# Kernel tuning notes

Hardware: AMD Instinct MI355X
Metric: run time of the kernel (lower is better)

Reference implementation:

```python
import jax, jax.numpy as jnp
import numpy as np

N_CLANS = 600   # rows of graph_fc.npy -> number of clan classes
MAX_F = 128     # max families per clan (padding size for stacked family heads)
B, L, D = 8192, 64, 256
NEG = -1e9      # mask value for padded family logits


def setup_inputs() -> dict:
    key = jax.random.key(0)
    k1, k2, k3, k4, k5, k6 = jax.random.split(key, 6)
    output = jax.random.normal(k1, (B, L, D), dtype=jnp.float32)
    fc = jax.random.randint(k2, (N_CLANS,), 1, MAX_F + 1)           # families per clan
    label_clan = jax.random.randint(k3, (B,), 0, N_CLANS)
    raw = jax.random.randint(k4, (B,), 0, MAX_F)
    label_family = raw % fc[label_clan]                              # valid family per sample
    W_clan = jax.random.normal(k5, (N_CLANS, D), dtype=jnp.float32) * 0.05
    b_clan = jnp.zeros((N_CLANS,), dtype=jnp.float32)
    W_fam = jax.random.normal(k6, (N_CLANS, MAX_F, D), dtype=jnp.float32) * 0.05
    b_fam = jnp.zeros((N_CLANS, MAX_F), dtype=jnp.float32)
    return {"output": output, "label_clan": label_clan, "label_family": label_family,
            "fc": fc, "W_clan": W_clan, "b_clan": b_clan, "W_fam": W_fam, "b_fam": b_fam}


def reference(output, label_clan, label_family, fc, W_clan, b_clan, W_fam, b_fam):
    x = output.mean(axis=1)                                          # [B, D]
    # clan CE loss (reduction='sum')
    logits_c = x @ W_clan.T + b_clan                                 # [B, N_CLANS]
    logp_c = jax.nn.log_softmax(logits_c, axis=-1)
    loss_clan = -jnp.take_along_axis(logp_c, label_clan[:, None], axis=1).sum()
    # routed per-sample family head: gather head weights by clan label
    Wg = W_fam[label_clan]                                           # [B, MAX_F, D]
    bg = b_fam[label_clan]                                           # [B, MAX_F]
    logits_f = jnp.einsum('bfd,bd->bf', Wg, x) + bg                  # [B, MAX_F]
    n_fam = fc[label_clan]                                           # [B]
    valid = jnp.arange(MAX_F)[None, :] < n_fam[:, None]              # mask padded families
    logits_f = jnp.where(valid, logits_f, NEG)
    logp_f = jax.nn.log_softmax(logits_f, axis=-1)
    nll = -jnp.take_along_axis(logp_f, label_family[:, None], axis=1)[:, 0]  # [B]
    active = n_fam > 1                                               # only clans with >1 family
    loss_family = jnp.where(active, nll, 0.0).sum()
    count = active.sum()
    loss = (loss_clan + loss_family) / (output.shape[0] + count)
    return loss
```

## Files before the change

kernel.cpp:

```cpp
#include <hip/hip_runtime.h>
#include <hip/hip_bf16.h>

#define B_SZ 8192
#define L_SZ 64
#define D_SZ 256
#define NC   600
#define MAXF 128
#define CAP  64

__global__ __launch_bounds__(256) void mean_kernel(const float* __restrict__ out,
                                                   float* __restrict__ x) {
    int gid = blockIdx.x * 256 + threadIdx.x;
    int b = gid >> 6, d4 = gid & 63;
    const float4* p = (const float4*)(out + (size_t)b * L_SZ * D_SZ) + d4;
    float4 acc = {0.f, 0.f, 0.f, 0.f};
#pragma unroll 8
    for (int l = 0; l < L_SZ; ++l) {
        float4 v = p[(size_t)l * (D_SZ / 4)];
        acc.x += v.x; acc.y += v.y; acc.z += v.z; acc.w += v.w;
    }
    const float s = 1.0f / 64.0f;
    acc.x *= s; acc.y *= s; acc.z *= s; acc.w *= s;
    ((float4*)(x + (size_t)b * D_SZ))[d4] = acc;
}

__global__ __launch_bounds__(256) void scatter_kernel(const int* __restrict__ label_clan,
                                                      const int* __restrict__ fc,
                                                      int* __restrict__ cnt,
                                                      int* __restrict__ list,
                                                      int* __restrict__ active_cnt) {
    int b = blockIdx.x * 256 + threadIdx.x;
    int cl = label_clan[b];
    int pos = atomicAdd(&cnt[cl], 1);
    if (pos < CAP) list[cl * CAP + pos] = b;
    int act = (fc[cl] > 1) ? 1 : 0;
    unsigned long long ball = __ballot(act);
    if ((threadIdx.x & 63) == 0) atomicAdd(active_cnt, (int)__popcll(ball));
}

#define CBM 32
__global__ __launch_bounds__(256) void clan_fused(const float* __restrict__ x,
                                                  const float* __restrict__ Wc,
                                                  const float* __restrict__ bc,
                                                  const int* __restrict__ label_clan,
                                                  float* __restrict__ acc_loss) {
    __shared__ float As[CBM][260];
    __shared__ float Bs[64][68];
    __shared__ float redm[CBM][16];
    __shared__ float mrow[CBM], srow[CBM], mnew[CBM], lablog[CBM];
    __shared__ int   labc[CBM];
    int t = threadIdx.x;
    int tx = t & 15, ty = t >> 4;
    int row0 = blockIdx.x * CBM;

#pragma unroll
    for (int rep = 0; rep < 8; ++rep) {
        int idx = t + rep * 256;
        int r = idx >> 6, c4 = idx & 63;
        *(float4*)&As[r][c4 * 4] = *(const float4*)(x + (size_t)(row0 + r) * D_SZ + c4 * 4);
    }
    if (t < CBM) {
        mrow[t] = -1e30f; srow[t] = 0.f; lablog[t] = 0.f;
        labc[t] = label_clan[row0 + t];
    }
    __syncthreads();

    for (int ct = 0; ct < 10; ++ct) {
        int c0 = ct * 64;
        float acc[2][4] = {};
        for (int k0 = 0; k0 < D_SZ; k0 += 64) {
            __syncthreads();
#pragma unroll
            for (int rep = 0; rep < 4; ++rep) {
                int idx = t + rep * 256;
                int col = idx >> 4, kq = idx & 15;
                int c = c0 + col;
                float4 v = {0.f, 0.f, 0.f, 0.f};
                if (c < NC) v = *(const float4*)(Wc + (size_t)c * D_SZ + k0 + kq * 4);
                *(float4*)&Bs[col][kq * 4] = v;
            }
            __syncthreads();
#pragma unroll
            for (int kk = 0; kk < 16; ++kk) {
                float4 a0 = *(float4*)&As[ty][k0 + kk * 4];
                float4 a1 = *(float4*)&As[ty + 16][k0 + kk * 4];
                float4 b[4];
#pragma unroll
                for (int j = 0; j < 4; ++j) b[j] = *(float4*)&Bs[tx + 16 * j][kk * 4];
#pragma unroll
                for (int j = 0; j < 4; ++j) {
                    acc[0][j] += a0.x * b[j].x + a0.y * b[j].y + a0.z * b[j].z + a0.w * b[j].w;
                    acc[1][j] += a1.x * b[j].x + a1.y * b[j].y + a1.z * b[j].z + a1.w * b[j].w;
                }
            }
        }
        float lg[2][4];
#pragma unroll
        for (int i = 0; i < 2; ++i) {
            int row = ty + 16 * i;
#pragma unroll
            for (int j = 0; j < 4; ++j) {
                int c = c0 + tx + 16 * j;
                float v = (c < NC) ? acc[i][j] + bc[c] : -1e30f;
                lg[i][j] = v;
                if (c < NC && c == labc[row]) lablog[row] = v;
            }
        }
#pragma unroll
        for (int i = 0; i < 2; ++i) {
            int row = ty + 16 * i;
            redm[row][tx] = fmaxf(fmaxf(lg[i][0], lg[i][1]), fmaxf(lg[i][2], lg[i][3]));
        }
        __syncthreads();
        if (t < CBM) {
            float tm = redm[t][0];
#pragma unroll
            for (int q = 1; q < 16; ++q) tm = fmaxf(tm, redm[t][q]);
            mnew[t] = fmaxf(mrow[t], tm);
        }
        __syncthreads();
#pragma unroll
        for (int i = 0; i < 2; ++i) {
            int row = ty + 16 * i;
            float mn = mnew[row];
            redm[row][tx] = __expf(lg[i][0] - mn) + __expf(lg[i][1] - mn)
                          + __expf(lg[i][2] - mn) + __expf(lg[i][3] - mn);
        }
        __syncthreads();
        if (t < CBM) {
            float s = 0.f;
#pragma unroll
            for (int q = 0; q < 16; ++q) s += redm[t][q];
            srow[t] = srow[t] * __expf(mrow[t] - mnew[t]) + s;
            mrow[t] = mnew[t];
        }
    }
    __syncthreads();
    if (t < 64) {
        float loss = 0.f;
        if (t < CBM) loss = __logf(srow[t]) + mrow[t] - lablog[t];
#pragma unroll
        for (int off = 16; off; off >>= 1) loss += __shfl_down(loss, off);
        if (t == 0) atomicAdd(acc_loss, loss);
    }
}

#define CHUNK 16
__global__ __launch_bounds__(256) void family_kernel(const float* __restrict__ x,
                                                     const float* __restrict__ Wf,
                                                     const float* __restrict__ bf,
                                                     const int* __restrict__ fc,
                                                     const int* __restrict__ cnt,
                                                     const int* __restrict__ list,
                                                     const int* __restrict__ label_family,
                                                     float* __restrict__ acc_loss) {
    int clan = blockIdx.x;
    int nf = fc[clan];
    if (nf <= 1) return;
    int n = min(cnt[clan], CAP);
    if (n == 0) return;
    __shared__ float sx[CHUNK][D_SZ];
    __shared__ float slog[CHUNK][MAXF];
    __shared__ int sb[CHUNK];
    __shared__ float wl[4];
    int t = threadIdx.x;
    int lane = t & 63, wid = t >> 6;
    const float* Wbase = Wf + (size_t)clan * MAXF * D_SZ;

    float wave_loss = 0.f;
    for (int s0 = 0; s0 < n; s0 += CHUNK) {
        int cn = min(CHUNK, n - s0);
        if (t < cn) sb[t] = list[clan * CAP + s0 + t];
        __syncthreads();
        for (int q = t; q < cn * (D_SZ / 4); q += 256) {
            int s = q >> 6, d4 = q & 63;
            ((float4*)sx[s])[d4] = ((const float4*)(x + (size_t)sb[s] * D_SZ))[d4];
        }
        __syncthreads();
        for (int f = wid; f < nf; f += 4) {
            float4 w = ((const float4*)(Wbase + (size_t)f * D_SZ))[lane];
            float bias = bf[clan * MAXF + f];
            for (int s = 0; s < cn; ++s) {
                float4 xv = ((float4*)sx[s])[lane];
                float p = w.x * xv.x + w.y * xv.y + w.z * xv.z + w.w * xv.w;
#pragma unroll
                for (int off = 32; off; off >>= 1) p += __shfl_down(p, off);
                if (lane == 0) slog[s][f] = p + bias;
            }
        }
        __syncthreads();
        for (int s = wid; s < cn; s += 4) {
            float v0 = (lane < nf) ? slog[s][lane] : -1e30f;
            float v1 = (lane + 64 < nf) ? slog[s][lane + 64] : -1e30f;
            float m = fmaxf(v0, v1);
#pragma unroll
            for (int off = 32; off; off >>= 1) m = fmaxf(m, __shfl_down(m, off));
            m = __shfl(m, 0);
            float e = 0.f;
            if (lane < nf) e += __expf(v0 - m);
            if (lane + 64 < nf) e += __expf(v1 - m);
#pragma unroll
            for (int off = 32; off; off >>= 1) e += __shfl_down(e, off);
            if (lane == 0) {
                int b = sb[s];
                int lf = label_family[b];
                wave_loss += __logf(e) + m - slog[s][lf];
            }
        }
        __syncthreads();
    }
    if (lane == 0) wl[wid] = wave_loss;
    __syncthreads();
    if (t == 0) {
        float v = wl[0] + wl[1] + wl[2] + wl[3];
        if (v != 0.f) atomicAdd(acc_loss, v);
    }
}

__global__ void finalize_kernel(const float* __restrict__ accs,
                                const int* __restrict__ active_cnt,
                                float* __restrict__ out) {
    out[0] = (accs[0] + accs[1]) / (8192.0f + (float)(*active_cnt));
}

extern "C" void kernel_launch(void* const* d_in, const int* in_sizes, int n_in,
                              void* d_out, int out_size, void* d_ws, size_t ws_size,
                              hipStream_t stream) {
    (void)in_sizes; (void)n_in; (void)out_size; (void)ws_size;
    const float* output       = (const float*)d_in[0];
    const int*   label_clan   = (const int*)d_in[1];
    const int*   label_family = (const int*)d_in[2];
    const int*   fc           = (const int*)d_in[3];
    const float* W_clan       = (const float*)d_in[4];
    const float* b_clan       = (const float*)d_in[5];
    const float* W_fam        = (const float*)d_in[6];
    const float* b_fam        = (const float*)d_in[7];
    float* out = (float*)d_out;

    char* ws = (char*)d_ws;
    const size_t OFF_X    = 0;
    const size_t OFF_CNT  = OFF_X + (size_t)B_SZ * D_SZ * 4;
    const size_t OFF_ACC  = OFF_CNT + 2560;
    const size_t OFF_LIST = OFF_ACC + 16;
    float* x      = (float*)(ws + OFF_X);
    int*   cnt    = (int*)(ws + OFF_CNT);
    float* accs   = (float*)(ws + OFF_ACC);
    int*   act    = (int*)(ws + OFF_ACC + 8);
    int*   list   = (int*)(ws + OFF_LIST);

    hipMemsetAsync(ws + OFF_CNT, 0, 2560 + 16, stream);

    mean_kernel<<<B_SZ * D_SZ / 4 / 256, 256, 0, stream>>>(output, x);
    scatter_kernel<<<B_SZ / 256, 256, 0, stream>>>(label_clan, fc, cnt, list, act);
    clan_fused<<<B_SZ / CBM, 256, 0, stream>>>(x, W_clan, b_clan, label_clan, accs);
    family_kernel<<<NC, 256, 0, stream>>>(x, W_fam, b_fam, fc, cnt, list, label_family, accs + 1);
    finalize_kernel<<<1, 1, 0, stream>>>(accs, act, out);
}
```

Before: 1.067 ms.

## Fuse scatter into mean kernel and run clan and family heads in one launch

```diff
diff --git a/kernel.cpp b/kernel.cpp
--- a/kernel.cpp
+++ b/kernel.cpp
@@ -7,10 +7,27 @@
 #define NC   600
 #define MAXF 128
 #define CAP  64
-
-__global__ __launch_bounds__(256) void mean_kernel(const float* __restrict__ out,
-                                                   float* __restrict__ x) {
-    int gid = blockIdx.x * 256 + threadIdx.x;
+#define CBM  32
+#define CHUNK 16
+
+__global__ __launch_bounds__(256) void mean_scatter(const float* __restrict__ out,
+                                                    float* __restrict__ x,
+                                                    const int* __restrict__ label_clan,
+                                                    const int* __restrict__ fc,
+                                                    int* __restrict__ cnt,
+                                                    int* __restrict__ list,
+                                                    int* __restrict__ active_cnt) {
+    int t = threadIdx.x;
+    if (blockIdx.x < 32) {
+        int b = blockIdx.x * 256 + t;
+        int cl = label_clan[b];
+        int pos = atomicAdd(&cnt[cl], 1);
+        if (pos < CAP) list[cl * CAP + pos] = b;
+        int act = (fc[cl] > 1) ? 1 : 0;
+        unsigned long long ball = __ballot(act);
+        if ((t & 63) == 0) atomicAdd(active_cnt, (int)__popcll(ball));
+    }
+    int gid = blockIdx.x * 256 + t;
     int b = gid >> 6, d4 = gid & 63;
     const float4* p = (const float4*)(out + (size_t)b * L_SZ * D_SZ) + d4;
     float4 acc = {0.f, 0.f, 0.f, 0.f};
@@ -24,34 +41,26 @@
     ((float4*)(x + (size_t)b * D_SZ))[d4] = acc;
 }
 
-__global__ __launch_bounds__(256) void scatter_kernel(const int* __restrict__ label_clan,
-                                                      const int* __restrict__ fc,
-                                                      int* __restrict__ cnt,
-                                                      int* __restrict__ list,
-                                                      int* __restrict__ active_cnt) {
-    int b = blockIdx.x * 256 + threadIdx.x;
-    int cl = label_clan[b];
-    int pos = atomicAdd(&cnt[cl], 1);
-    if (pos < CAP) list[cl * CAP + pos] = b;
-    int act = (fc[cl] > 1) ? 1 : 0;
-    unsigned long long ball = __ballot(act);
-    if ((threadIdx.x & 63) == 0) atomicAdd(active_cnt, (int)__popcll(ball));
-}
-
-#define CBM 32
-__global__ __launch_bounds__(256) void clan_fused(const float* __restrict__ x,
-                                                  const float* __restrict__ Wc,
-                                                  const float* __restrict__ bc,
-                                                  const int* __restrict__ label_clan,
-                                                  float* __restrict__ acc_loss) {
-    __shared__ float As[CBM][260];
-    __shared__ float Bs[64][68];
-    __shared__ float redm[CBM][16];
-    __shared__ float mrow[CBM], srow[CBM], mnew[CBM], lablog[CBM];
-    __shared__ int   labc[CBM];
+#define SMEM_FLOATS (53376 / 4)
+
+__device__ void clan_branch(float* smem, int blk,
+                            const float* __restrict__ x,
+                            const float* __restrict__ Wc,
+                            const float* __restrict__ bc,
+                            const int* __restrict__ label_clan,
+                            float* __restrict__ acc_loss) {
+    float (*As)[260] = (float(*)[260])smem;
+    float (*Bs)[68]  = (float(*)[68])(smem + 32 * 260);
+    float (*redm)[16] = (float(*)[16])(smem + 32 * 260 + 64 * 68);
+    float* mrow   = smem + 32 * 260 + 64 * 68 + 32 * 16;
+    float* srow   = mrow + 32;
+    float* mnew   = srow + 32;
+    float* lablog = mnew + 32;
+    int*   labc   = (int*)(lablog + 32);
+
     int t = threadIdx.x;
     int tx = t & 15, ty = t >> 4;
-    int row0 = blockIdx.x * CBM;
+    int row0 = blk * CBM;
 
 #pragma unroll
     for (int rep = 0; rep < 8; ++rep) {
@@ -145,24 +154,24 @@
     }
 }
 
-#define CHUNK 16
-__global__ __launch_bounds__(256) void family_kernel(const float* __restrict__ x,
-                                                     const float* __restrict__ Wf,
-                                                     const float* __restrict__ bf,
-                                                     const int* __restrict__ fc,
-                                                     const int* __restrict__ cnt,
-                                                     const int* __restrict__ list,
-                                                     const int* __restrict__ label_family,
-                                                     float* __restrict__ acc_loss) {
-    int clan = blockIdx.x;
+__device__ void family_branch(float* smem, int clan,
+                              const float* __restrict__ x,
+                              const float* __restrict__ Wf,
+                              const float* __restrict__ bf,
+                              const int* __restrict__ fc,
+                              const int* __restrict__ cnt,
+                              const int* __restrict__ list,
+                              const int* __restrict__ label_family,
+                              float* __restrict__ acc_loss) {
     int nf = fc[clan];
     if (nf <= 1) return;
     int n = min(cnt[clan], CAP);
     if (n == 0) return;
-    __shared__ float sx[CHUNK][D_SZ];
-    __shared__ float slog[CHUNK][MAXF];
-    __shared__ int sb[CHUNK];
-    __shared__ float wl[4];
+    float (*sx)[D_SZ]   = (float(*)[D_SZ])smem;
+    float (*slog)[MAXF] = (float(*)[MAXF])(smem + CHUNK * D_SZ);
+    int*   sb = (int*)(smem + CHUNK * D_SZ + CHUNK * MAXF);
+    float* wl = (float*)(sb + CHUNK);
+
     int t = threadIdx.x;
     int lane = t & 63, wid = t >> 6;
     const float* Wbase = Wf + (size_t)clan * MAXF * D_SZ;
@@ -214,6 +223,25 @@
     if (t == 0) {
         float v = wl[0] + wl[1] + wl[2] + wl[3];
         if (v != 0.f) atomicAdd(acc_loss, v);
+    }
+}
+
+__global__ __launch_bounds__(256) void clan_family(const float* __restrict__ x,
+                                                   const float* __restrict__ Wc,
+                                                   const float* __restrict__ bc,
+                                                   const int* __restrict__ label_clan,
+                                                   const float* __restrict__ Wf,
+                                                   const float* __restrict__ bf,
+                                                   const int* __restrict__ fc,
+                                                   const int* __restrict__ cnt,
+                                                   const int* __restrict__ list,
+                                                   const int* __restrict__ label_family,
+                                                   float* __restrict__ accs) {
+    __shared__ float smem[SMEM_FLOATS];
+    if (blockIdx.x < 256) {
+        clan_branch(smem, blockIdx.x, x, Wc, bc, label_clan, accs);
+    } else {
+        family_branch(smem, blockIdx.x - 256, x, Wf, bf, fc, cnt, list, label_family, accs + 1);
     }
 }
 
@@ -250,9 +278,9 @@
 
     hipMemsetAsync(ws + OFF_CNT, 0, 2560 + 16, stream);
 
-    mean_kernel<<<B_SZ * D_SZ / 4 / 256, 256, 0, stream>>>(output, x);
-    scatter_kernel<<<B_SZ / 256, 256, 0, stream>>>(label_clan, fc, cnt, list, act);
-    clan_fused<<<B_SZ / CBM, 256, 0, stream>>>(x, W_clan, b_clan, label_clan, accs);
-    family_kernel<<<NC, 256, 0, stream>>>(x, W_fam, b_fam, fc, cnt, list, label_family, accs + 1);
+    mean_scatter<<<B_SZ * D_SZ / 4 / 256, 256, 0, stream>>>(output, x, label_clan, fc,
+                                                            cnt, list, act);
+    clan_family<<<256 + NC, 256, 0, stream>>>(x, W_clan, b_clan, label_clan,
+                                              W_fam, b_fam, fc, cnt, list, label_family, accs);
     finalize_kernel<<<1, 1, 0, stream>>>(accs, act, out);
 }
```

Measured after the change: 1.015 ms. -4.8%, faster.
